# Performance work log

Measured on AMD Instinct MI355X. Metric: run time of the kernel, lower is better.

Reference implementation:

```python
import jax, jax.numpy as jnp
import numpy as np

B, N, V, J, K = 2, 16384, 10475, 55, 6
WEIGHT_STD2 = 2.0 * 0.1 ** 2  # 0.02


def setup_inputs() -> dict:
    ks = jax.random.split(jax.random.key(0), 5)
    x = jax.random.normal(ks[0], (B, N, 3), dtype=jnp.float32)
    # cam = [scale, tx, ty]; scale kept positive/near 1
    scale = jax.random.uniform(ks[1], (B, 1), minval=0.8, maxval=1.2)
    trans = jax.random.normal(ks[1], (B, 2)) * 0.05
    cam = jnp.concatenate([scale, trans], axis=-1).astype(jnp.float32)
    # skinning weights: sparse-ish simplex rows
    lbs_weights = jax.nn.softmax(4.0 * jax.random.normal(ks[2], (V, J)), axis=-1).astype(jnp.float32)
    # per-vertex rigid-ish transforms: identity + noise
    verts_transform = (jnp.eye(4, dtype=jnp.float32)[None, None]
                       + 0.1 * jax.random.normal(ks[3], (B, V, 4, 4), dtype=jnp.float32))
    posed_verts = jax.random.normal(ks[4], (B, V, 3), dtype=jnp.float32)
    return {"x": x, "cam": cam, "lbs_weights": lbs_weights,
            "verts_transform": verts_transform, "posed_verts": posed_verts}


def _orth_proj_inv(x, cam):
    # inverse of batch_orth_proj: undo scale, undo xy translation
    scale = cam[:, 0].reshape(-1, 1, 1)
    t = cam[:, 1:3].reshape(-1, 1, 2)
    xy = x[..., :2] / scale - t
    z = x[..., 2:] / scale
    return jnp.concatenate([xy, z], axis=-1)


def _knn(points, verts, k):
    # brute-force KNN on squared euclidean distance (matches knn_points)
    p2 = jnp.sum(points * points, axis=-1, keepdims=True)          # [B,N,1]
    v2 = jnp.sum(verts * verts, axis=-1)                           # [B,V]
    cross = jnp.einsum('bnd,bvd->bnv', points, verts)              # [B,N,V]
    d2 = p2 + v2[:, None, :] - 2.0 * cross
    neg_d, idx = jax.lax.top_k(-d2, k)                             # smallest k
    return jnp.maximum(-neg_d, 0.0), idx


def reference(x, cam, lbs_weights, verts_transform, posed_verts):
    posed_x = _orth_proj_inv(x, cam)                               # [B,N,3]

    # KNN is under torch.no_grad in the original
    dists, idx = _knn(jax.lax.stop_gradient(posed_x),
                      jax.lax.stop_gradient(posed_verts), K)       # [B,N,K]

    # gather skinning weights of neighbors: lbs_weights shared across batch
    w_nb = lbs_weights[idx]                                        # [B,N,K,J]
    conf = jnp.exp(-jnp.sum(jnp.abs(w_nb - w_nb[..., 0:1, :]), axis=-1) / WEIGHT_STD2)
    conf = (conf > 0.9).astype(posed_x.dtype)                      # [B,N,K]

    w = jnp.exp(-dists) * conf
    w = w / jnp.sum(w, axis=-1, keepdims=True)                     # [B,N,K]

    # batched gather of per-vertex transforms
    T_nb = jax.vmap(lambda T, i: T[i])(verts_transform, idx)       # [B,N,K,4,4]
    x_transform = jnp.einsum('bnk,bnkij->bnij', w, T_nb)           # [B,N,4,4]

    # batch_transform: apply rigid transform to posed points
    cano_x = (jnp.einsum('bnij,bnj->bni', x_transform[..., :3, :3], posed_x)
              + x_transform[..., :3, 3])                           # [B,N,3]
    return cano_x
```

## Files before the change

kernel.cpp:

```cpp
#include <hip/hip_runtime.h>
#include <math.h>

#define B_ 2
#define N_ 16384
#define V_ 10475
#define J_ 55
#define K_ 6

constexpr int   NB      = 512;
constexpr int   SSTRIDE = 16384;
constexpr float ZLO     = -6.0f;
constexpr float ZHI     =  6.0f;
constexpr float HBIN    = (ZHI - ZLO) / (float)NB;
constexpr float INVH    = (float)NB / (ZHI - ZLO);

__device__ __forceinline__ int zbin(float z) {
    int b = (int)floorf((z - ZLO) * INVH);
    return min(max(b, 0), NB - 1);
}

__device__ __forceinline__ double shfl_d(double v, int src) {
    int lo = __double2loint(v), hi = __double2hiint(v);
    lo = __shfl(lo, src, 64);
    hi = __shfl(hi, src, 64);
    return __hiloint2double(hi, lo);
}

__global__ __launch_bounds__(1024) void build_kernel(const float* __restrict__ pverts,
                                                     const float* __restrict__ x,
                                                     const float* __restrict__ cam,
                                                     float4* __restrict__ pvs,
                                                     int* __restrict__ vidx,
                                                     int* __restrict__ psort,
                                                     int* __restrict__ binStartV) {
    __shared__ int hist[NB];
    __shared__ int cur[NB];
    const int t = threadIdx.x;
    const int b = blockIdx.x >> 1;
    const bool vertsKind = (blockIdx.x & 1) == 0;

    if (t < NB) hist[t] = 0;
    __syncthreads();

    if (vertsKind) {
        for (int i = t; i < V_; i += 1024)
            atomicAdd(&hist[zbin(pverts[((size_t)(b * V_ + i)) * 3 + 2])], 1);
    } else {
        const float cs = cam[b * 3 + 0];
        for (int i = t; i < N_; i += 1024)
            atomicAdd(&hist[zbin(x[((size_t)(b * N_ + i)) * 3 + 2] / cs)], 1);
    }
    __syncthreads();

    for (int off = 1; off < NB; off <<= 1) {
        int v = 0;
        if (t < NB && t >= off) v = hist[t - off];
        __syncthreads();
        if (t < NB) hist[t] += v;
        __syncthreads();
    }
    if (t < NB) {
        int ex = (t == 0) ? 0 : hist[t - 1];
        cur[t] = ex;
        if (vertsKind) binStartV[b * (NB + 1) + t] = ex;
    }
    if (vertsKind && t == 0) binStartV[b * (NB + 1) + NB] = hist[NB - 1];
    __syncthreads();

    if (vertsKind) {
        for (int i = t; i < V_; i += 1024) {
            size_t g = (size_t)(b * V_ + i) * 3;
            float vx = pverts[g], vy = pverts[g + 1], vz = pverts[g + 2];
            int pos = atomicAdd(&cur[zbin(vz)], 1);
            pvs[b * SSTRIDE + pos] = make_float4(vx, vy, vz, vx * vx + vy * vy + vz * vz);
            vidx[b * SSTRIDE + pos] = i;
        }
    } else {
        const float cs = cam[b * 3 + 0];
        for (int i = t; i < N_; i += 1024) {
            float z = x[((size_t)(b * N_ + i)) * 3 + 2] / cs;
            int pos = atomicAdd(&cur[zbin(z)], 1);
            psort[b * N_ + pos] = b * N_ + i;
        }
    }
}

__global__ __launch_bounds__(1024, 4) void knn_kernel(const float4* __restrict__ pvs,
                                                      const int* __restrict__ vidx,
                                                      const int* __restrict__ binStartV,
                                                      const int* __restrict__ psort,
                                                      const float* __restrict__ x,
                                                      const float* __restrict__ cam,
                                                      const float* __restrict__ lbs,
                                                      const float* __restrict__ vt,
                                                      float* __restrict__ out) {
    __shared__ float4 tile[2048];
    __shared__ unsigned int cK[16][64][6];
    __shared__ unsigned int eK[64][8];
    __shared__ float gateG;

    const int tid = threadIdx.x, lane = tid & 63, wid = tid >> 6;
    const int b   = blockIdx.x >> 8;
    const int blk = blockIdx.x & 255;
    const int pid = psort[b * N_ + blk * 64 + lane];

    const float cs = cam[b * 3 + 0], ctx = cam[b * 3 + 1], cty = cam[b * 3 + 2];
    const float Px = x[pid * 3 + 0] / cs - ctx;
    const float Py = x[pid * 3 + 1] / cs - cty;
    const float Pz = x[pid * 3 + 2] / cs;
    const float Ax = -2.f * Px, Ay = -2.f * Py, Az = -2.f * Pz;
    const float Cc = Px * Px + Py * Py + Pz * Pz + 1.0e-4f;

    float zmin = Pz, zmax = Pz;
#pragma unroll
    for (int m = 1; m <= 32; m <<= 1) {
        zmin = fminf(zmin, __shfl_xor(zmin, m, 64));
        zmax = fmaxf(zmax, __shfl_xor(zmax, m, 64));
    }

    const int* bs = binStartV + b * (NB + 1);
    int cbin = zbin(0.5f * (zmin + zmax));
    int center = (bs[cbin] + bs[cbin + 1]) >> 1;
    int lo = center - 1024;
    lo = max(0, min(lo, V_ - 2048));
    int hi = lo + 2048;

    unsigned int bK[6];
#pragma unroll
    for (int t = 0; t < 6; ++t) bK[t] = 0xFFFFFFFFu;

    const float4* pb = pvs + b * SSTRIDE;

#define SCAN_RANGE(RL, CNT)                                                    \
    for (int i = wid; i < (CNT); i += 16) {                                    \
        float4 q = tile[i];                  \
        float d2 = fmaf(Ax, q.x, fmaf(Ay, q.y, fmaf(Az, q.z, Cc + q.w)));      \
        unsigned int key = (__float_as_uint(d2) & 0xFFFFC000u)                 \
                         | (unsigned int)((RL) + i);                           \
        if (key < bK[5]) {                                                     \
            unsigned int kk = key;                                             \
            _Pragma("unroll")                                                  \
            for (int t = 0; t < 6; ++t) {                                      \
                unsigned int mn = min(kk, bK[t]);                              \
                kk = max(kk, bK[t]);                                           \
                bK[t] = mn;                                                    \
            }                                                                  \
        }                                                                      \
    }

    tile[tid]        = pb[lo + tid];
    tile[tid + 1024] = pb[lo + 1024 + tid];
    __syncthreads();
    SCAN_RANGE(lo, 2048)

#pragma unroll
    for (int t = 0; t < 6; ++t) cK[wid][lane][t] = bK[t];
    __syncthreads();
    if (wid == 0) {
        unsigned int U[6];
#pragma unroll
        for (int t = 0; t < 6; ++t) U[t] = 0xFFFFFFFFu;
        for (int ss = 0; ss < 16; ++ss)
#pragma unroll
            for (int t = 0; t < 6; ++t) {
                unsigned int kk = cK[ss][lane][t];
                if (kk < U[5]) {
#pragma unroll
                    for (int u = 0; u < 6; ++u) {
                        unsigned int mn = min(kk, U[u]);
                        kk = max(kk, U[u]);
                        U[u] = mn;
                    }
                }
            }
        float g = __uint_as_float(U[5] | 0x3FFFu);
#pragma unroll
        for (int m = 1; m <= 32; m <<= 1)
            g = fmaxf(g, __shfl_xor(g, m, 64));
        if (lane == 0) gateG = g;
    }
    __syncthreads();
    const float G = gateG;

    while (true) {
        float bl = 3.0e38f, br = 3.0e38f;
        if (lo > 0) {
            int j = zbin(pb[lo - 1].z);
            bl = (j >= NB - 1) ? 0.f
               : fmaxf(0.f, zmin - (ZLO + (float)(j + 1) * HBIN));
        }
        if (hi < V_) {
            int j = zbin(pb[hi].z);
            br = (j <= 0) ? 0.f
               : fmaxf(0.f, (ZLO + (float)j * HBIN) - zmax);
        }
        bool canL = (lo > 0)  && (bl * bl < G);
        bool canR = (hi < V_) && (br * br < G);
        if (!canL && !canR) break;
        bool left = canL && (!canR || bl <= br);
        int rl, rh;
        if (left) { rh = lo; rl = max(0, lo - 1024); lo = rl; }
        else      { rl = hi; rh = min(V_, hi + 1024); hi = rh; }
        __syncthreads();
        int cnt = rh - rl;
        if (tid < cnt) tile[tid] = pb[rl + tid];
        __syncthreads();
        SCAN_RANGE(rl, cnt)
    }
#undef SCAN_RANGE

    __syncthreads();
#pragma unroll
    for (int t = 0; t < 6; ++t) cK[wid][lane][t] = bK[t];
    __syncthreads();
    if (wid == 0) {
        unsigned int E[8];
#pragma unroll
        for (int t = 0; t < 8; ++t) E[t] = 0xFFFFFFFFu;
        for (int ss = 0; ss < 16; ++ss)
#pragma unroll
            for (int t = 0; t < 6; ++t) {
                unsigned int kk = cK[ss][lane][t];
                if (kk < E[7]) {
#pragma unroll
                    for (int u = 0; u < 8; ++u) {
                        unsigned int mn = min(kk, E[u]);
                        kk = max(kk, E[u]);
                        E[u] = mn;
                    }
                }
            }
#pragma unroll
        for (int t = 0; t < 8; ++t) eK[lane][t] = E[t];
    }
    __syncthreads();

    const int lj = lane & 15;
    const int gb = lane & ~15;
    const int pl = (wid << 2) + (lane >> 4);
    const int pid2 = psort[b * N_ + blk * 64 + pl];

    const float Qx = x[pid2 * 3 + 0] / cs - ctx;
    const float Qy = x[pid2 * 3 + 1] / cs - cty;
    const float Qz = x[pid2 * 3 + 2] / cs;

    double myd = 1.0e300;
    int mygi = 0x7FFFFFFF;
    if (lj < 8) {
        unsigned int key = eK[pl][lj];
        if (key != 0xFFFFFFFFu) {
            int pos = (int)(key & 0x3FFFu);
            mygi = vidx[b * SSTRIDE + pos];
            float4 vq = pb[pos];
            const double csd = (double)cs;
            const double PX = (double)x[pid2 * 3 + 0] / csd - (double)ctx;
            const double PY = (double)x[pid2 * 3 + 1] / csd - (double)cty;
            const double PZ = (double)x[pid2 * 3 + 2] / csd;
            double vx = (double)vq.x, vy = (double)vq.y, vz = (double)vq.z;
            double v2 = vx * vx + vy * vy + vz * vz;
            double P2 = PX * PX + PY * PY + PZ * PZ;
            double dot = PX * vx + PY * vy + PZ * vz;
            myd = P2 + v2 - 2.0 * dot;
        }
    }
    double dd[8];
    int ii[8];
#pragma unroll
    for (int t = 0; t < 8; ++t) { dd[t] = shfl_d(myd, gb + t); ii[t] = __shfl(mygi, gb + t, 64); }
#define CE_(a, c) { \
        bool sw_ = (dd[a] > dd[c]) || (dd[a] == dd[c] && ii[a] > ii[c]); \
        double dt_ = sw_ ? dd[a] : dd[c]; dd[a] = sw_ ? dd[c] : dd[a]; dd[c] = dt_; \
        int it_ = sw_ ? ii[a] : ii[c]; ii[a] = sw_ ? ii[c] : ii[a]; ii[c] = it_; }
#pragma unroll
    for (int r = 0; r < 4; ++r) {
        CE_(0, 1) CE_(2, 3) CE_(4, 5) CE_(6, 7)
        CE_(1, 2) CE_(3, 4) CE_(5, 6)
    }
#undef CE_

    const int i0 = (ii[0] < V_) ? ii[0] : 0;
    float r0v[4];
#pragma unroll
    for (int r = 0; r < 4; ++r) {
        int e = lj + (r << 4);
        r0v[r] = (e < J_) ? lbs[i0 * J_ + e] : 0.f;
    }
    float wgt[K_];
    wgt[0] = expf(-fmaxf((float)dd[0], 0.f));
#pragma unroll
    for (int k = 1; k < K_; ++k) {
        int gk = (ii[k] < V_) ? ii[k] : 0;
        float sv = 0.f;
#pragma unroll
        for (int r = 0; r < 4; ++r) {
            int e = lj + (r << 4);
            sv += (e < J_) ? fabsf(lbs[gk * J_ + e] - r0v[r]) : 0.f;
        }
#pragma unroll
        for (int m = 1; m <= 8; m <<= 1) sv += __shfl_xor(sv, m, 64);
        wgt[k] = (sv < 0.0021072103f) ? expf(-fmaxf((float)dd[k], 0.f)) : 0.f;
    }
    float wsum = ((wgt[0] + wgt[1]) + (wgt[2] + wgt[3])) + (wgt[4] + wgt[5]);
    float inv = 1.f / wsum;

    float acc = 0.f;
#pragma unroll
    for (int k = 0; k < K_; ++k) {
        int gk = (ii[k] < V_) ? ii[k] : 0;
        acc += (wgt[k] * inv) * vt[((size_t)(b * V_ + gk)) * 16 + lj];
    }
    const int c = lj & 3;
    float pc = (c == 0) ? Qx : (c == 1) ? Qy : (c == 2) ? Qz : 1.f;
    float part = acc * pc;
    part += __shfl_xor(part, 1, 64);
    part += __shfl_xor(part, 2, 64);
    if (lj == 0)      out[pid2 * 3 + 0] = part;
    else if (lj == 4) out[pid2 * 3 + 1] = part;
    else if (lj == 8) out[pid2 * 3 + 2] = part;
}

extern "C" void kernel_launch(void* const* d_in, const int* in_sizes, int n_in,
                              void* d_out, int out_size, void* d_ws, size_t ws_size,
                              hipStream_t stream) {
    const float* x      = (const float*)d_in[0];
    const float* cam    = (const float*)d_in[1];
    const float* lbs    = (const float*)d_in[2];
    const float* vt     = (const float*)d_in[3];
    const float* pverts = (const float*)d_in[4];
    float* out = (float*)d_out;

    char* ws = (char*)d_ws;
    int* binStartV = (int*)ws;
    float4* pvs = (float4*)(ws + 4112);
    int* vidx  = (int*)((char*)pvs + (size_t)B_ * SSTRIDE * 16);
    int* psort = vidx + B_ * SSTRIDE;

    build_kernel<<<4, 1024, 0, stream>>>(pverts, x, cam, pvs, vidx, psort, binStartV);
    knn_kernel<<<B_ * (N_ / 64), 1024, 0, stream>>>(pvs, vidx, binStartV, psort,
                                                    x, cam, lbs, vt, out);
}
```

Measured before the change: 230.4 us.

## Parallelize per-point top-k merge across wavefronts and use async global-to-LDS loads

Replaces the single-wavefront serial merge of 16 per-wave candidate lists with a butterfly bitonic merge spread across all 16 wavefronts. Each point's lists are handled by 16 lanes that exchange through shuffles, and the gate is reduced through a small shared array. Tile loads now use global_load_lds async copies instead of register round-trips, padding counts to 64. The launch-bounds occupancy hint rises from 4 to 8, which may force register spilling. The padded async loads can also read past the valid range.

```diff
diff --git a/kernel.cpp b/kernel.cpp
--- a/kernel.cpp
+++ b/kernel.cpp
@@ -24,6 +24,12 @@
     lo = __shfl(lo, src, 64);
     hi = __shfl(hi, src, 64);
     return __hiloint2double(hi, lo);
+}
+
+__device__ __forceinline__ void async16(void* lds, const void* g) {
+    __builtin_amdgcn_global_load_lds(
+        (const __attribute__((address_space(1))) void*)g,
+        (__attribute__((address_space(3))) void*)lds, 16, 0, 0);
 }
 
 __global__ __launch_bounds__(1024) void build_kernel(const float* __restrict__ pverts,
@@ -85,7 +91,7 @@
     }
 }
 
-__global__ __launch_bounds__(1024, 4) void knn_kernel(const float4* __restrict__ pvs,
+__global__ __launch_bounds__(1024, 8) void knn_kernel(const float4* __restrict__ pvs,
                                                       const int* __restrict__ vidx,
                                                       const int* __restrict__ binStartV,
                                                       const int* __restrict__ psort,
@@ -96,8 +102,7 @@
                                                       float* __restrict__ out) {
     __shared__ float4 tile[2048];
     __shared__ unsigned int cK[16][64][6];
-    __shared__ unsigned int eK[64][8];
-    __shared__ float gateG;
+    __shared__ float sMax[16];
 
     const int tid = threadIdx.x, lane = tid & 63, wid = tid >> 6;
     const int b   = blockIdx.x >> 8;
@@ -148,39 +153,50 @@
         }                                                                      \
     }
 
-    tile[tid]        = pb[lo + tid];
-    tile[tid + 1024] = pb[lo + 1024 + tid];
+#define PMERGE(E)                                                              \
+    {                                                                          \
+        const int pj = lane & 15, pp = (wid << 2) + (lane >> 4);               \
+        _Pragma("unroll")                                                      \
+        for (int t = 0; t < 6; ++t) (E)[t] = cK[pj][pp][t];                    \
+        (E)[6] = 0xFFFFFFFFu; (E)[7] = 0xFFFFFFFFu;                            \
+        _Pragma("unroll")                                                      \
+        for (int s = 1; s <= 8; s <<= 1) {                                     \
+            unsigned int Bt[8], Cv[8];                                         \
+            _Pragma("unroll")                                                  \
+            for (int t = 0; t < 8; ++t)                                        \
+                Bt[t] = (unsigned int)__shfl_xor((int)(E)[t], s, 64);          \
+            _Pragma("unroll")                                                  \
+            for (int t = 0; t < 8; ++t) Cv[t] = min((E)[t], Bt[7 - t]);        \
+            CEU(0, 4) CEU(1, 5) CEU(2, 6) CEU(3, 7)                            \
+            CEU(0, 2) CEU(1, 3) CEU(4, 6) CEU(5, 7)                            \
+            CEU(0, 1) CEU(2, 3) CEU(4, 5) CEU(6, 7)                            \
+            _Pragma("unroll")                                                  \
+            for (int t = 0; t < 8; ++t) (E)[t] = Cv[t];                        \
+        }                                                                      \
+    }
+#define CEU(a, c) { unsigned int mn_ = min(Cv[a], Cv[c]); Cv[c] = max(Cv[a], Cv[c]); Cv[a] = mn_; }
+
+    async16(&tile[tid], &pb[lo + tid]);
+    async16(&tile[tid + 1024], &pb[lo + 1024 + tid]);
     __syncthreads();
     SCAN_RANGE(lo, 2048)
 
 #pragma unroll
     for (int t = 0; t < 6; ++t) cK[wid][lane][t] = bK[t];
     __syncthreads();
-    if (wid == 0) {
-        unsigned int U[6];
-#pragma unroll
-        for (int t = 0; t < 6; ++t) U[t] = 0xFFFFFFFFu;
-        for (int ss = 0; ss < 16; ++ss)
-#pragma unroll
-            for (int t = 0; t < 6; ++t) {
-                unsigned int kk = cK[ss][lane][t];
-                if (kk < U[5]) {
-#pragma unroll
-                    for (int u = 0; u < 6; ++u) {
-                        unsigned int mn = min(kk, U[u]);
-                        kk = max(kk, U[u]);
-                        U[u] = mn;
-                    }
-                }
-            }
-        float g = __uint_as_float(U[5] | 0x3FFFu);
+    {
+        unsigned int E1[8];
+        PMERGE(E1)
+        float g = __uint_as_float(E1[5] | 0x3FFFu);
 #pragma unroll
         for (int m = 1; m <= 32; m <<= 1)
             g = fmaxf(g, __shfl_xor(g, m, 64));
-        if (lane == 0) gateG = g;
-    }
-    __syncthreads();
-    const float G = gateG;
+        if (lane == 0) sMax[wid] = g;
+    }
+    __syncthreads();
+    float G = sMax[0];
+#pragma unroll
+    for (int t = 1; t < 16; ++t) G = fmaxf(G, sMax[t]);
 
     while (true) {
         float bl = 3.0e38f, br = 3.0e38f;
@@ -203,7 +219,8 @@
         else      { rl = hi; rh = min(V_, hi + 1024); hi = rh; }
         __syncthreads();
         int cnt = rh - rl;
-        if (tid < cnt) tile[tid] = pb[rl + tid];
+        int cntPad = (cnt + 63) & ~63;
+        if (tid < cntPad) async16(&tile[tid], &pb[rl + tid]);
         __syncthreads();
         SCAN_RANGE(rl, cnt)
     }
@@ -213,27 +230,10 @@
 #pragma unroll
     for (int t = 0; t < 6; ++t) cK[wid][lane][t] = bK[t];
     __syncthreads();
-    if (wid == 0) {
-        unsigned int E[8];
-#pragma unroll
-        for (int t = 0; t < 8; ++t) E[t] = 0xFFFFFFFFu;
-        for (int ss = 0; ss < 16; ++ss)
-#pragma unroll
-            for (int t = 0; t < 6; ++t) {
-                unsigned int kk = cK[ss][lane][t];
-                if (kk < E[7]) {
-#pragma unroll
-                    for (int u = 0; u < 8; ++u) {
-                        unsigned int mn = min(kk, E[u]);
-                        kk = max(kk, E[u]);
-                        E[u] = mn;
-                    }
-                }
-            }
-#pragma unroll
-        for (int t = 0; t < 8; ++t) eK[lane][t] = E[t];
-    }
-    __syncthreads();
+    unsigned int E[8];
+    PMERGE(E)
+#undef PMERGE
+#undef CEU
 
     const int lj = lane & 15;
     const int gb = lane & ~15;
@@ -247,7 +247,7 @@
     double myd = 1.0e300;
     int mygi = 0x7FFFFFFF;
     if (lj < 8) {
-        unsigned int key = eK[pl][lj];
+        unsigned int key = E[lj];
         if (key != 0xFFFFFFFFu) {
             int pos = (int)(key & 0x3FFFu);
             mygi = vidx[b * SSTRIDE + pos];
```

Measured after the change: 221.3 us. -3.9%, faster.
